# Performance work log

Hardware: AMD Instinct MI355X
Metric: run time of the kernel (lower is better)

Reference implementation:

```python
import jax, jax.numpy as jnp
import numpy as np

M, N, NUM_ITER, BATCH = 512, 2048, 16, 4096


def setup_inputs() -> dict:
    key = jax.random.key(0)
    k_y, k_D, k_thr = jax.random.split(key, 3)
    # Dictionary D (== A in the module), column-scaled like a sensing matrix
    D = np.asarray(jax.random.normal(k_D, (M, N), dtype=jnp.float32)) / np.sqrt(M)
    # W = inv(D D^T) D, then normalize columns so w_i . d_i == 1 (ALISTA analytic weight)
    W = np.linalg.inv(D @ D.T) @ D
    W = W / np.sum(W * D, axis=0, keepdims=True)
    y = jax.random.normal(k_y, (BATCH, M), dtype=jnp.float32)
    thr = jax.random.uniform(k_thr, (NUM_ITER,), dtype=jnp.float32) * 0.1  # positive thresholds
    step = jnp.ones((NUM_ITER,), dtype=jnp.float32)
    return {"y": y, "A": jnp.asarray(D), "W": jnp.asarray(W), "thr": thr, "step": step}


def reference(y, A, W, thr, step):
    # y: [B, m]; A, W: [m, n]; thr, step: [numIter]
    B = y.shape[0]
    n = A.shape[1]

    def body(d, ts):
        t, s = ts
        r = d @ A.T - y                      # [B, m]  == (A @ d.T - y.T).T
        z = d - s * (r @ W)                  # [B, n]  == (W.T @ r.T).T
        d_new = jnp.sign(z) * jnp.maximum(jnp.abs(z) - t, 0.0)  # soft threshold
        return d_new, d_new

    d0 = jnp.zeros((B, n), dtype=y.dtype)
    _, xs = jax.lax.scan(body, d0, (thr, step))
    return xs  # [numIter, B, n]: all intermediate iterates, like the returned list x
```

## Files before the change

kernel.cpp:

```cpp
#include <hip/hip_runtime.h>


#define NDIM 2048
#define MDIM 512
#define BATCHN 4096
#define NITER 16
#define BM 128
#define BN 128
#define BK 64

#define BM2 256
#define BN2 128
#define BK2 32
#define NKT (NDIM / BK2)

typedef _Float16 f16;
typedef f16 f16x8 __attribute__((ext_vector_type(8)));
typedef float f32x4 __attribute__((ext_vector_type(4)));

__device__ __forceinline__ void gload_lds16(const void* g, void* lds) {
  __builtin_amdgcn_global_load_lds(
      (const __attribute__((address_space(1))) unsigned int*)g,
      (__attribute__((address_space(3))) unsigned int*)lds, 16, 0, 0);
}

__global__ __launch_bounds__(512, 2) void alista_iter_gemm(
    const f16* __restrict__ Ds, const f16* __restrict__ P,
    const f16* __restrict__ Ch,
    const float* __restrict__ thr, const float* __restrict__ step, int it,
    float sigma, float inv_sigma, float inv_sigma_next,
    float* __restrict__ outIter, f16* __restrict__ DsNext)
{
  __shared__ __align__(16) f16 ldsA[4 * BM2 * BK2];
  __shared__ __align__(16) f16 ldsB[4 * BN2 * BK2];

  const int tid = threadIdx.x;
  const int w = tid >> 6, l = tid & 63;
  const int wm = w >> 1, wn = w & 1;
  const int h = l >> 4;

  const int bid = blockIdx.x;
  const int wgid = (bid & 7) * 32 + (bid >> 3);
  const int rowTile = (wgid >> 4) * BM2;
  const int colTile = (wgid & 15) * BN2;

  const f16* Abase = Ds + (size_t)rowTile * NDIM;
  const f16* Bbase = P + (size_t)colTile * NDIM;

  auto stage = [&](int t) {
    const int buf = t & 3;
#pragma unroll
    for (int r = 0; r < 2; ++r) {
      int row = r * 128 + (tid >> 2);
      int colb = ((tid & 3) << 4) ^ (((row >> 1) & 3) << 4);
      gload_lds16((const char*)(Abase + (size_t)row * NDIM + t * BK2) + colb,
                  (char*)ldsA + buf * 16384 + r * 8192 + w * 1024);
    }
    {
      int row = tid >> 2;
      int colb = ((tid & 3) << 4) ^ (((row >> 1) & 3) << 4);
      gload_lds16((const char*)(Bbase + (size_t)row * NDIM + t * BK2) + colb,
                  (char*)ldsB + buf * 8192 + w * 1024);
    }
  };

#define READ_FRAGS(t, af, bf)                                                   \
  {                                                                             \
    const f16* bA_ = ldsA + ((t) & 3) * 8192;                                   \
    const f16* bB_ = ldsB + ((t) & 3) * 4096;                                   \
    _Pragma("unroll")                                                           \
    for (int m = 0; m < 4; ++m) {                                               \
      int row = wm * 64 + m * 16 + (l & 15);                                    \
      af[m] = *(const f16x8*)(bA_ + row * 32 + ((h ^ ((row >> 1) & 3)) << 3));  \
    }                                                                           \
    _Pragma("unroll")                                                           \
    for (int n = 0; n < 4; ++n) {                                               \
      int row = wn * 64 + n * 16 + (l & 15);                                    \
      bf[n] = *(const f16x8*)(bB_ + row * 32 + ((h ^ ((row >> 1) & 3)) << 3));  \
    }                                                                           \
  }

#define MFMA_CLUSTER(af, bf)                                                    \
  __builtin_amdgcn_s_setprio(1);                                                \
  _Pragma("unroll")                                                             \
  for (int m = 0; m < 4; ++m)                                                   \
    _Pragma("unroll")                                                           \
    for (int n = 0; n < 4; ++n)                                                 \
      acc[m][n] = __builtin_amdgcn_mfma_f32_16x16x32_f16(af[m], bf[n],          \
                                                         acc[m][n], 0, 0, 0);   \
  __builtin_amdgcn_s_setprio(0);

  stage(0);
  stage(1);
  asm volatile("s_waitcnt vmcnt(3)" ::: "memory");
  __builtin_amdgcn_s_barrier();

  f32x4 acc[4][4] = {};
  f16x8 afE[4], bfE[4], afO[4], bfO[4];

  READ_FRAGS(0, afE, bfE);
  stage(2);
  asm volatile("s_waitcnt vmcnt(3)" ::: "memory");
  __builtin_amdgcn_s_barrier();
  __builtin_amdgcn_sched_barrier(0);

  for (int t = 0; t < NKT; t += 2) {
    READ_FRAGS(t + 1, afO, bfO);
    if (t + 3 < NKT) stage(t + 3);
    __builtin_amdgcn_sched_barrier(0);
    MFMA_CLUSTER(afE, bfE);
    if (t + 3 < NKT) asm volatile("s_waitcnt vmcnt(3)" ::: "memory");
    else             asm volatile("s_waitcnt vmcnt(0)" ::: "memory");
    __builtin_amdgcn_s_barrier();
    __builtin_amdgcn_sched_barrier(0);

    if (t + 2 < NKT) READ_FRAGS(t + 2, afE, bfE);
    if (t + 4 < NKT) stage(t + 4);
    __builtin_amdgcn_sched_barrier(0);
    MFMA_CLUSTER(afO, bfO);
    if (t + 4 < NKT) asm volatile("s_waitcnt vmcnt(3)" ::: "memory");
    else             asm volatile("s_waitcnt vmcnt(0)" ::: "memory");
    __builtin_amdgcn_s_barrier();
    __builtin_amdgcn_sched_barrier(0);
  }

  const int baseRow = rowTile + wm * 64 + (h << 2);
  const int baseCol = colTile + wn * 64 + (l & 15);
  const float s = step[it];
  const float tt = thr[it];
  const size_t itOff = (size_t)it * (size_t)BATCHN * NDIM;
#pragma unroll
  for (int m = 0; m < 4; ++m)
#pragma unroll
    for (int n = 0; n < 4; ++n)
#pragma unroll
      for (int r = 0; r < 4; ++r) {
        int row = baseRow + m * 16 + r;
        int col = baseCol + n * 16;
        size_t g = (size_t)row * NDIM + col;
        float v = acc[m][n][r];
        float ds = (float)Ds[g];
        float cv = (float)Ch[g];
        float z = sigma * (ds - s * (v - cv * inv_sigma));
        float az = __builtin_fabsf(z) - tt;
        float dn = az > 0.f ? (z > 0.f ? az : -az) : 0.f;
        outIter[itOff + g] = dn;
        DsNext[g] = (f16)(dn * inv_sigma_next);
      }
#undef READ_FRAGS
#undef MFMA_CLUSTER
}

__global__ __launch_bounds__(256, 2) void gemm_pre(
    const f16* __restrict__ Ap, const f16* __restrict__ Bp, int K,
    f16* __restrict__ outH)
{
  __shared__ __align__(16) f16 ldsA[BM * BK];
  __shared__ __align__(16) f16 ldsB[BN * BK];
  int t = threadIdx.x;
  int w = t >> 6, l = t & 63;
  int wr = w >> 1, wc = w & 1;
  int rowTile = blockIdx.y * BM;
  int colTile = blockIdx.x * BN;

  f32x4 acc[4][4] = {};
  const f16* Arow = Ap + (size_t)rowTile * K;
  const f16* Brow = Bp + (size_t)colTile * K;
  for (int kt = 0; kt < K; kt += BK) {
    __syncthreads();
#pragma unroll
    for (int n = 0; n < 4; ++n) {
      int e = n * 2048 + t * 8;
      int r = e >> 6, c = e & 63;
      gload_lds16(Arow + (size_t)r * K + kt + c, (char*)ldsA + n * 4096 + w * 1024);
    }
#pragma unroll
    for (int n = 0; n < 4; ++n) {
      int e = n * 2048 + t * 8;
      int r = e >> 6, c = e & 63;
      gload_lds16(Brow + (size_t)r * K + kt + c, (char*)ldsB + n * 4096 + w * 1024);
    }
    asm volatile("s_waitcnt vmcnt(0)" ::: "memory");
    __syncthreads();
#pragma unroll
    for (int ks = 0; ks < 2; ++ks) {
      f16x8 a[4], b[4];
#pragma unroll
      for (int m = 0; m < 4; ++m)
        a[m] = *(const f16x8*)(ldsA + ((wr * 64 + m * 16 + (l & 15)) * BK + ks * 32 + (l >> 4) * 8));
#pragma unroll
      for (int n = 0; n < 4; ++n)
        b[n] = *(const f16x8*)(ldsB + ((wc * 64 + n * 16 + (l & 15)) * BK + ks * 32 + (l >> 4) * 8));
#pragma unroll
      for (int m = 0; m < 4; ++m)
#pragma unroll
        for (int n = 0; n < 4; ++n)
          acc[m][n] = __builtin_amdgcn_mfma_f32_16x16x32_f16(a[m], b[n], acc[m][n], 0, 0, 0);
    }
  }

  int baseRow = rowTile + wr * 64 + ((l >> 4) << 2);
  int baseCol = colTile + wc * 64 + (l & 15);
#pragma unroll
  for (int m = 0; m < 4; ++m)
#pragma unroll
    for (int n = 0; n < 4; ++n)
#pragma unroll
      for (int r = 0; r < 4; ++r) {
        size_t g = (size_t)(baseRow + m * 16 + r) * NDIM + baseCol + n * 16;
        outH[g] = (f16)acc[m][n][r];
      }
}

__global__ __launch_bounds__(256) void trans_h(
    const float* __restrict__ in, f16* __restrict__ oh)
{
  __shared__ float tile[64][65];
  int t = threadIdx.x;
  int tr = t >> 6;
  int tc = t & 63;
  int r0 = blockIdx.y * 64;
  int c0 = blockIdx.x * 64;
#pragma unroll
  for (int i = 0; i < 16; ++i) {
    int r = i * 4 + tr;
    tile[r][tc] = in[(size_t)(r0 + r) * NDIM + c0 + tc];
  }
  __syncthreads();
#pragma unroll
  for (int i = 0; i < 16; ++i) {
    int r = i * 4 + tr;
    oh[(size_t)(c0 + r) * MDIM + r0 + tc] = (f16)tile[tc][r];
  }
}

__global__ __launch_bounds__(256) void tofp16(
    const float* __restrict__ in, f16* __restrict__ oh)
{
  size_t i = (size_t)blockIdx.x * 256 + threadIdx.x;
  oh[i] = (f16)in[i];
}

__global__ __launch_bounds__(256) void alista_iter0(
    const f16* __restrict__ Ch, const float* __restrict__ thr,
    const float* __restrict__ step, float* __restrict__ out, f16* __restrict__ Ds1)
{
  size_t i = (size_t)blockIdx.x * 256 + threadIdx.x;
  float s = step[0], tt = thr[0];
  float z = s * (float)Ch[i];
  float az = __builtin_fabsf(z) - tt;
  float dn = az > 0.f ? (z > 0.f ? az : -az) : 0.f;
  out[i] = dn;
  Ds1[i] = (f16)dn;
}

extern "C" void kernel_launch(void* const* d_in, const int* in_sizes, int n_in,
                              void* d_out, int out_size, void* d_ws, size_t ws_size,
                              hipStream_t stream)
{
  const float* y    = (const float*)d_in[0];
  const float* A    = (const float*)d_in[1];
  const float* W    = (const float*)d_in[2];
  const float* thr  = (const float*)d_in[3];
  const float* step = (const float*)d_in[4];
  float* out = (float*)d_out;
  char* ws = (char*)d_ws;

  f16* Pht = (f16*)(ws + 0);
  f16* Ch  = (f16*)(ws + (8ull  << 20));
  f16* DsA = (f16*)(ws + (24ull << 20));
  f16* DsB = (f16*)(ws + (40ull << 20));
  f16* Wth = (f16*)(ws + (24ull << 20));
  f16* Ath = (f16*)(ws + (26ull << 20));
  f16* yh  = (f16*)(ws + (40ull << 20));

  trans_h<<<dim3(32, 8), 256, 0, stream>>>(A, Ath);
  trans_h<<<dim3(32, 8), 256, 0, stream>>>(W, Wth);
  tofp16<<<(BATCHN * MDIM) / 256, 256, 0, stream>>>(y, yh);

  gemm_pre<<<dim3(16, 16), 256, 0, stream>>>(Wth, Ath, MDIM, Pht);
  gemm_pre<<<dim3(16, 32), 256, 0, stream>>>(yh, Wth, MDIM, Ch);

  alista_iter0<<<(BATCHN * NDIM) / 256, 256, 0, stream>>>(Ch, thr, step, out, DsA);

  f16* cur = DsA;
  f16* nxt = DsB;
  float sigma = 1.0f;
  for (int it = 1; it < NITER; ++it) {
    alista_iter_gemm<<<dim3(256), 512, 0, stream>>>(
        cur, Pht, Ch, thr, step, it,
        sigma, 1.0f / sigma, 0.25f / sigma, out, nxt);
    sigma *= 4.0f;
    f16* tmp = cur; cur = nxt; nxt = tmp;
  }
}
```

Before: 788.6 us.

## Load B fragments directly from global to registers, bypass LDS for B

The iteration GEMM stops staging the B operand (P) through LDS. Each wave now loads its B fragments straight from global memory into registers, while A keeps the LDS pipeline. The vmcnt waits are retuned to cover the extra outstanding loads, and the block-to-tile mapping is changed to a grouped swizzle meant to improve L2 locality. This frees LDS and removes one set of LDS writes and reads, but B data is now fetched redundantly by the four waves sharing a column, and the loads are less coalesced (16-byte chunks strided by rows).

```diff
diff --git a/kernel.cpp b/kernel.cpp
--- a/kernel.cpp
+++ b/kernel.cpp
@@ -32,7 +32,6 @@
     float* __restrict__ outIter, f16* __restrict__ DsNext)
 {
   __shared__ __align__(16) f16 ldsA[4 * BM2 * BK2];
-  __shared__ __align__(16) f16 ldsB[4 * BN2 * BK2];
 
   const int tid = threadIdx.x;
   const int w = tid >> 6, l = tid & 63;
@@ -40,9 +39,10 @@
   const int h = l >> 4;
 
   const int bid = blockIdx.x;
-  const int wgid = (bid & 7) * 32 + (bid >> 3);
-  const int rowTile = (wgid >> 4) * BM2;
-  const int colTile = (wgid & 15) * BN2;
+  const int x = bid & 7;
+  const int q = bid >> 3;
+  const int rowTile = ((x >> 1) * 4 + (q >> 3)) * BM2;
+  const int colTile = ((x & 1) * 8 + (q & 7)) * BN2;
 
   const f16* Abase = Ds + (size_t)rowTile * NDIM;
   const f16* Bbase = P + (size_t)colTile * NDIM;
@@ -54,29 +54,26 @@
       int row = r * 128 + (tid >> 2);
       int colb = ((tid & 3) << 4) ^ (((row >> 1) & 3) << 4);
       gload_lds16((const char*)(Abase + (size_t)row * NDIM + t * BK2) + colb,
-                  (char*)ldsA + buf * 16384 + r * 8192 + w * 1024);
-    }
-    {
-      int row = tid >> 2;
-      int colb = ((tid & 3) << 4) ^ (((row >> 1) & 3) << 4);
-      gload_lds16((const char*)(Bbase + (size_t)row * NDIM + t * BK2) + colb,
-                  (char*)ldsB + buf * 8192 + w * 1024);
+                  (char*)ldsA + buf * 16384 + r * 8192 + tid * 16);
     }
   };
 
-#define READ_FRAGS(t, af, bf)                                                   \
+#define READ_A(t, af)                                                           \
   {                                                                             \
     const f16* bA_ = ldsA + ((t) & 3) * 8192;                                   \
-    const f16* bB_ = ldsB + ((t) & 3) * 4096;                                   \
     _Pragma("unroll")                                                           \
     for (int m = 0; m < 4; ++m) {                                               \
       int row = wm * 64 + m * 16 + (l & 15);                                    \
       af[m] = *(const f16x8*)(bA_ + row * 32 + ((h ^ ((row >> 1) & 3)) << 3));  \
     }                                                                           \
+  }
+
+#define BLOAD(t, bf)                                                            \
+  {                                                                             \
     _Pragma("unroll")                                                           \
     for (int n = 0; n < 4; ++n) {                                               \
       int row = wn * 64 + n * 16 + (l & 15);                                    \
-      bf[n] = *(const f16x8*)(bB_ + row * 32 + ((h ^ ((row >> 1) & 3)) << 3));  \
+      bf[n] = *(const f16x8*)(Bbase + (size_t)row * NDIM + (t) * BK2 + h * 8);  \
     }                                                                           \
   }
 
@@ -90,37 +87,46 @@
                                                          acc[m][n], 0, 0, 0);   \
   __builtin_amdgcn_s_setprio(0);
 
+  f32x4 acc[4][4] = {};
+  f16x8 afE[4], bfE[4], afO[4], bfO[4];
+
   stage(0);
   stage(1);
-  asm volatile("s_waitcnt vmcnt(3)" ::: "memory");
+  BLOAD(0, bfE);
+  asm volatile("s_waitcnt vmcnt(6)" ::: "memory");
   __builtin_amdgcn_s_barrier();
-
-  f32x4 acc[4][4] = {};
-  f16x8 afE[4], bfE[4], afO[4], bfO[4];
-
-  READ_FRAGS(0, afE, bfE);
+  READ_A(0, afE);
   stage(2);
-  asm volatile("s_waitcnt vmcnt(3)" ::: "memory");
+  asm volatile("s_waitcnt vmcnt(6)" ::: "memory");
   __builtin_amdgcn_s_barrier();
   __builtin_amdgcn_sched_barrier(0);
 
   for (int t = 0; t < NKT; t += 2) {
-    READ_FRAGS(t + 1, afO, bfO);
+    BLOAD(t + 1, bfO);
+    READ_A(t + 1, afO);
     if (t + 3 < NKT) stage(t + 3);
     __builtin_amdgcn_sched_barrier(0);
     MFMA_CLUSTER(afE, bfE);
-    if (t + 3 < NKT) asm volatile("s_waitcnt vmcnt(3)" ::: "memory");
-    else             asm volatile("s_waitcnt vmcnt(0)" ::: "memory");
-    __builtin_amdgcn_s_barrier();
+    if (t + 3 < NKT) {
+      asm volatile("s_waitcnt vmcnt(6)" ::: "memory");
+      __builtin_amdgcn_s_barrier();
+    } else if (t + 2 < NKT) {
+      asm volatile("s_waitcnt vmcnt(4)" ::: "memory");
+      __builtin_amdgcn_s_barrier();
+    }
     __builtin_amdgcn_sched_barrier(0);
 
-    if (t + 2 < NKT) READ_FRAGS(t + 2, afE, bfE);
+    if (t + 2 < NKT) { BLOAD(t + 2, bfE); READ_A(t + 2, afE); }
     if (t + 4 < NKT) stage(t + 4);
     __builtin_amdgcn_sched_barrier(0);
     MFMA_CLUSTER(afO, bfO);
-    if (t + 4 < NKT) asm volatile("s_waitcnt vmcnt(3)" ::: "memory");
-    else             asm volatile("s_waitcnt vmcnt(0)" ::: "memory");
-    __builtin_amdgcn_s_barrier();
+    if (t + 4 < NKT) {
+      asm volatile("s_waitcnt vmcnt(6)" ::: "memory");
+      __builtin_amdgcn_s_barrier();
+    } else if (t + 3 < NKT) {
+      asm volatile("s_waitcnt vmcnt(4)" ::: "memory");
+      __builtin_amdgcn_s_barrier();
+    }
     __builtin_amdgcn_sched_barrier(0);
   }
 
@@ -147,7 +153,8 @@
         outIter[itOff + g] = dn;
         DsNext[g] = (f16)(dn * inv_sigma_next);
       }
-#undef READ_FRAGS
+#undef READ_A
+#undef BLOAD
 #undef MFMA_CLUSTER
 }
 
```

Measured after the change: 1.431 ms. 81.5% more time.

## Restructure iteration GEMM to 3-stage BK=64 pipeline with split prefetch

Applied to the files above, without the earlier changes.

Switches the main per-iteration GEMM from a 4-buffer K=32 pipeline to a 3-buffer K=64 pipeline with an 8-chunk XOR swizzle. Each K tile is consumed in two halves, and the prefetch of tile t+2 is split across them. Fragment double-buffering is replaced by a single fragment set with explicit lgkmcnt waits and extra barriers. The aim is fewer loop iterations and barriers per unit of work and larger loads. The cost is more shared memory per block (144KB vs 128KB), which may hurt the 2-blocks-per-CU occupancy, and the single fragment set serializes LDS reads with the MFMAs.

```diff
diff --git a/kernel.cpp b/kernel.cpp
--- a/kernel.cpp
+++ b/kernel.cpp
@@ -11,8 +11,8 @@
 
 #define BM2 256
 #define BN2 128
-#define BK2 32
-#define NKT (NDIM / BK2)
+#define BK3 64
+#define NK3 (NDIM / BK3)
 
 typedef _Float16 f16;
 typedef f16 f16x8 __attribute__((ext_vector_type(8)));
@@ -31,8 +31,8 @@
     float sigma, float inv_sigma, float inv_sigma_next,
     float* __restrict__ outIter, f16* __restrict__ DsNext)
 {
-  __shared__ __align__(16) f16 ldsA[4 * BM2 * BK2];
-  __shared__ __align__(16) f16 ldsB[4 * BN2 * BK2];
+  __shared__ __align__(16) f16 ldsA[3 * BM2 * BK3];
+  __shared__ __align__(16) f16 ldsB[3 * BN2 * BK3];
 
   const int tid = threadIdx.x;
   const int w = tid >> 6, l = tid & 63;
@@ -47,40 +47,37 @@
   const f16* Abase = Ds + (size_t)rowTile * NDIM;
   const f16* Bbase = P + (size_t)colTile * NDIM;
 
-  auto stage = [&](int t) {
-    const int buf = t & 3;
-#pragma unroll
-    for (int r = 0; r < 2; ++r) {
-      int row = r * 128 + (tid >> 2);
-      int colb = ((tid & 3) << 4) ^ (((row >> 1) & 3) << 4);
-      gload_lds16((const char*)(Abase + (size_t)row * NDIM + t * BK2) + colb,
-                  (char*)ldsA + buf * 16384 + r * 8192 + w * 1024);
-    }
-    {
-      int row = tid >> 2;
-      int colb = ((tid & 3) << 4) ^ (((row >> 1) & 3) << 4);
-      gload_lds16((const char*)(Bbase + (size_t)row * NDIM + t * BK2) + colb,
-                  (char*)ldsB + buf * 8192 + w * 1024);
-    }
+  auto stageA = [&](int buf, int t, int r) {
+    int row = r * 64 + (tid >> 3);
+    int gsw = ((tid & 7) ^ (row & 7)) << 4;
+    gload_lds16((const char*)(Abase + (size_t)row * NDIM + t * BK3) + gsw,
+                (char*)ldsA + buf * 32768 + r * 8192 + w * 1024);
   };
-
-#define READ_FRAGS(t, af, bf)                                                   \
+  auto stageB = [&](int buf, int t, int r) {
+    int row = r * 64 + (tid >> 3);
+    int gsw = ((tid & 7) ^ (row & 7)) << 4;
+    gload_lds16((const char*)(Bbase + (size_t)row * NDIM + t * BK3) + gsw,
+                (char*)ldsB + buf * 16384 + r * 8192 + w * 1024);
+  };
+
+#define READ8(bR, kh, af, bf)                                                   \
   {                                                                             \
-    const f16* bA_ = ldsA + ((t) & 3) * 8192;                                   \
-    const f16* bB_ = ldsB + ((t) & 3) * 4096;                                   \
+    const f16* bA_ = ldsA + (bR) * 16384;                                       \
+    const f16* bB_ = ldsB + (bR) * 8192;                                        \
+    const int c_ = (kh) * 4 + h;                                                \
     _Pragma("unroll")                                                           \
     for (int m = 0; m < 4; ++m) {                                               \
       int row = wm * 64 + m * 16 + (l & 15);                                    \
-      af[m] = *(const f16x8*)(bA_ + row * 32 + ((h ^ ((row >> 1) & 3)) << 3));  \
+      af[m] = *(const f16x8*)(bA_ + row * 64 + ((c_ ^ (row & 7)) << 3));        \
     }                                                                           \
     _Pragma("unroll")                                                           \
     for (int n = 0; n < 4; ++n) {                                               \
       int row = wn * 64 + n * 16 + (l & 15);                                    \
-      bf[n] = *(const f16x8*)(bB_ + row * 32 + ((h ^ ((row >> 1) & 3)) << 3));  \
+      bf[n] = *(const f16x8*)(bB_ + row * 64 + ((c_ ^ (row & 7)) << 3));        \
     }                                                                           \
   }
 
-#define MFMA_CLUSTER(af, bf)                                                    \
+#define MFMA16(af, bf)                                                          \
   __builtin_amdgcn_s_setprio(1);                                                \
   _Pragma("unroll")                                                             \
   for (int m = 0; m < 4; ++m)                                                   \
@@ -90,38 +87,48 @@
                                                          acc[m][n], 0, 0, 0);   \
   __builtin_amdgcn_s_setprio(0);
 
-  stage(0);
-  stage(1);
-  asm volatile("s_waitcnt vmcnt(3)" ::: "memory");
-  __builtin_amdgcn_s_barrier();
-
   f32x4 acc[4][4] = {};
-  f16x8 afE[4], bfE[4], afO[4], bfO[4];
-
-  READ_FRAGS(0, afE, bfE);
-  stage(2);
-  asm volatile("s_waitcnt vmcnt(3)" ::: "memory");
+  f16x8 af[4], bf[4];
+
+#pragma unroll
+  for (int r = 0; r < 4; ++r) stageA(0, 0, r);
+#pragma unroll
+  for (int r = 0; r < 2; ++r) stageB(0, 0, r);
+#pragma unroll
+  for (int r = 0; r < 4; ++r) stageA(1, 1, r);
+#pragma unroll
+  for (int r = 0; r < 2; ++r) stageB(1, 1, r);
+  asm volatile("s_waitcnt vmcnt(6)" ::: "memory");
   __builtin_amdgcn_s_barrier();
   __builtin_amdgcn_sched_barrier(0);
 
-  for (int t = 0; t < NKT; t += 2) {
-    READ_FRAGS(t + 1, afO, bfO);
-    if (t + 3 < NKT) stage(t + 3);
+  int bR = 0;
+  int bS = 2;
+
+  for (int t = 0; t < NK3; ++t) {
+    const bool pf = (t + 2 < NK3);
+
+    READ8(bR, 0, af, bf);
+    if (pf) { stageA(bS, t + 2, 0); stageA(bS, t + 2, 1); stageB(bS, t + 2, 0); }
+    __builtin_amdgcn_s_barrier();
+    asm volatile("s_waitcnt lgkmcnt(0)" ::: "memory");
     __builtin_amdgcn_sched_barrier(0);
-    MFMA_CLUSTER(afE, bfE);
-    if (t + 3 < NKT) asm volatile("s_waitcnt vmcnt(3)" ::: "memory");
-    else             asm volatile("s_waitcnt vmcnt(0)" ::: "memory");
+    MFMA16(af, bf);
+    __builtin_amdgcn_s_barrier();
+
+    READ8(bR, 1, af, bf);
+    if (pf) { stageA(bS, t + 2, 2); stageA(bS, t + 2, 3); stageB(bS, t + 2, 1); }
+    __builtin_amdgcn_s_barrier();
+    asm volatile("s_waitcnt lgkmcnt(0)" ::: "memory");
+    __builtin_amdgcn_sched_barrier(0);
+    MFMA16(af, bf);
+    if (pf) asm volatile("s_waitcnt vmcnt(6)" ::: "memory");
+    else    asm volatile("s_waitcnt vmcnt(0)" ::: "memory");
     __builtin_amdgcn_s_barrier();
     __builtin_amdgcn_sched_barrier(0);
 
-    if (t + 2 < NKT) READ_FRAGS(t + 2, afE, bfE);
-    if (t + 4 < NKT) stage(t + 4);
-    __builtin_amdgcn_sched_barrier(0);
-    MFMA_CLUSTER(afO, bfO);
-    if (t + 4 < NKT) asm volatile("s_waitcnt vmcnt(3)" ::: "memory");
-    else             asm volatile("s_waitcnt vmcnt(0)" ::: "memory");
-    __builtin_amdgcn_s_barrier();
-    __builtin_amdgcn_sched_barrier(0);
+    bR = (bR == 2) ? 0 : bR + 1;
+    bS = (bS == 2) ? 0 : bS + 1;
   }
 
   const int baseRow = rowTile + wm * 64 + (h << 2);
@@ -147,8 +154,8 @@
         outIter[itOff + g] = dn;
         DsNext[g] = (f16)(dn * inv_sigma_next);
       }
-#undef READ_FRAGS
-#undef MFMA_CLUSTER
+#undef READ8
+#undef MFMA16
 }
 
 __global__ __launch_bounds__(256, 2) void gemm_pre(
```

Result: faster. 750.8 us (-4.8%).
